# Kernel tuning notes

Measured on AMD Instinct MI355X. Metric: run time of the kernel, lower is better.

Reference implementation:

```python
import jax, jax.numpy as jnp
import numpy as np

NEG_BIG = -9e15

def setup_inputs() -> dict:
    key = jax.random.key(0)
    k1, k2, k3, k4 = jax.random.split(key, 4)
    N, Fin, Fout = 8192, 256, 128
    x = jax.random.normal(k1, (N, Fin), dtype=jnp.float32)
    adj = jax.random.randint(k2, (N, N), 0, 2, dtype=jnp.int32)
    # xavier-uniform-like init
    limW = float(np.sqrt(6.0 / (Fin + Fout)))
    W = jax.random.uniform(k3, (Fin, Fout), minval=-limW, maxval=limW, dtype=jnp.float32)
    lima = float(np.sqrt(6.0 / (2 * Fout + 1)))
    a = jax.random.uniform(k4, (2 * Fout, 1), minval=-lima, maxval=lima, dtype=jnp.float32)
    return {"x": x, "adj": adj, "W": W, "a": a}

def reference(x, adj, W, a, alpha=0.2):
    # h: (N, Fout)
    h = x @ W
    Fout = W.shape[1]
    # Split a into source/target halves: e[i,j] = leakyrelu(h_i·a1 + h_j·a2)
    a1, a2 = a[:Fout, 0], a[Fout:, 0]
    s = h @ a1  # (N,) row (source) scores
    t = h @ a2  # (N,) col (target) scores
    e = jax.nn.leaky_relu(s[:, None] + t[None, :], negative_slope=alpha)  # (N, N)
    e = jnp.where(adj > 0, e, NEG_BIG)
    attention = jax.nn.softmax(e, axis=1)
    # dropout omitted (eval mode / training=False)
    return attention @ h
```

## Files before the change

kernel.cpp:

```cpp
#include <hip/hip_runtime.h>
#include <hip/hip_bf16.h>

typedef __attribute__((ext_vector_type(8))) short short8;
typedef __attribute__((ext_vector_type(4))) short short4v;
typedef __attribute__((ext_vector_type(4))) float f32x4;

#define NR 8192
#define LOG2E 1.4426950408889634f

__device__ __forceinline__ short f2bf(float f) {
  return __builtin_bit_cast(short, __float2bfloat16(f));
}

__global__ __launch_bounds__(256) void k_gemm_h(const float* __restrict__ x,
                                                const float* __restrict__ W,
                                                const float* __restrict__ a,
                                                short* __restrict__ HT2,
                                                float* __restrict__ sv,
                                                float* __restrict__ tv) {
  __shared__ short WT[128][136];
  const int tid = threadIdx.x;
  const int w = tid >> 6;
  const int L = tid & 63;
  const int lm = L & 15;
  const int q = L >> 4;
  const int i0 = blockIdx.x * 64;

  f32x4 acc[8];
#pragma unroll
  for (int nn = 0; nn < 8; ++nn) acc[nn] = (f32x4){0.f, 0.f, 0.f, 0.f};

  for (int kc = 0; kc < 256; kc += 128) {
    if (kc) __syncthreads();
#pragma unroll
    for (int p = 0; p < 16; ++p) {
      int idx = p * 256 + tid;
      int k = idx >> 5;
      int f4 = (idx & 31) * 4;
      float4 v = *(const float4*)&W[(kc + k) * 128 + f4];
      WT[f4 + 0][k] = f2bf(v.x);
      WT[f4 + 1][k] = f2bf(v.y);
      WT[f4 + 2][k] = f2bf(v.z);
      WT[f4 + 3][k] = f2bf(v.w);
    }
    __syncthreads();
#pragma unroll
    for (int ks = 0; ks < 4; ++ks) {
      int row = i0 + 16 * w + lm;
      const float* xp = &x[(size_t)row * 256 + kc + ks * 32 + q * 8];
      float4 xa = *(const float4*)xp;
      float4 xb = *(const float4*)(xp + 4);
      short8 af;
      af[0] = f2bf(xa.x); af[1] = f2bf(xa.y); af[2] = f2bf(xa.z); af[3] = f2bf(xa.w);
      af[4] = f2bf(xb.x); af[5] = f2bf(xb.y); af[6] = f2bf(xb.z); af[7] = f2bf(xb.w);
#pragma unroll
      for (int nn = 0; nn < 8; ++nn) {
        short8 bf = *(const short8*)&WT[nn * 16 + lm][ks * 32 + q * 8];
        acc[nn] = __builtin_amdgcn_mfma_f32_16x16x32_bf16(af, bf, acc[nn], 0, 0, 0);
      }
    }
  }

  const int ib = i0 + 16 * w + 4 * q;
  const int tbase = (ib >> 5) * 4096 + (ib & 31);
  float a1v[8], a2v[8];
#pragma unroll
  for (int nn = 0; nn < 8; ++nn) {
    a1v[nn] = a[nn * 16 + lm];
    a2v[nn] = a[128 + nn * 16 + lm];
  }
  float sr[4] = {0.f, 0.f, 0.f, 0.f};
  float tr[4] = {0.f, 0.f, 0.f, 0.f};
#pragma unroll
  for (int nn = 0; nn < 8; ++nn) {
    int f = nn * 16 + lm;
    short4v o;
    o[0] = f2bf(acc[nn][0]);
    o[1] = f2bf(acc[nn][1]);
    o[2] = f2bf(acc[nn][2]);
    o[3] = f2bf(acc[nn][3]);
    *(short4v*)&HT2[tbase + f * 32] = o;
#pragma unroll
    for (int r = 0; r < 4; ++r) {
      sr[r] += acc[nn][r] * a1v[nn];
      tr[r] += acc[nn][r] * a2v[nn];
    }
  }
#pragma unroll
  for (int d = 1; d < 16; d <<= 1) {
#pragma unroll
    for (int r = 0; r < 4; ++r) {
      sr[r] += __shfl_xor(sr[r], d);
      tr[r] += __shfl_xor(tr[r], d);
    }
  }
  if (lm == 0) {
#pragma unroll
    for (int r = 0; r < 4; ++r) {
      sv[ib + r] = sr[r] * LOG2E;
      tv[ib + r] = tr[r] * LOG2E;
    }
  }
}

__global__ __launch_bounds__(512, 4) void k_flash(const int* __restrict__ adj,
                                                  const short* __restrict__ HT2,
                                                  const float* __restrict__ sv,
                                                  const float* __restrict__ tv,
                                                  float* __restrict__ part,
                                                  float* __restrict__ lpart) {
  __shared__ short lds_s[32768];
  unsigned* ldsw = (unsigned*)lds_s;
  const int tid = threadIdx.x;
  const int w = tid >> 6;
  const int L = tid & 63;
  const int lm = L & 15;
  const int q = L >> 4;
  const int sp = blockIdx.x & 7;
  const int it = blockIdx.x >> 3;
  const int i0 = it * 128;

  const int row0 = i0 + 16 * w + lm;
  const float s0 = sv[row0];
  const size_t ar0 = (size_t)row0 * NR;

  f32x4 acc[8];
#pragma unroll
  for (int nn = 0; nn < 8; ++nn) acc[nn] = (f32x4){0.f, 0.f, 0.f, 0.f};
  float l0 = 0.f;

  const int tile0 = sp * 32;
  int jb = tile0 * 32 + q * 8;
  int4 sa00 = *(const int4*)&adj[ar0 + jb];
  int4 sa01 = *(const int4*)&adj[ar0 + jb + 4];

  for (int t = 0; t < 32; ++t) {
    if ((t & 7) == 0) {
      __syncthreads();
      const int pbase_t = tile0 + t;
#pragma unroll
      for (int z = 0; z < 8; ++z) {
        int id = z * 512 + tid;
        int tt = id >> 9;
        int k = id & 511;
        int f = k >> 2, c = k & 3;
        uint4 v = *(const uint4*)&HT2[(size_t)(pbase_t + tt) * 4096 + k * 8];
        int cs = c ^ ((f >> 1) & 3);
        *(uint4*)&ldsw[tt * 2048 + f * 16 + cs * 4] = v;
      }
      __syncthreads();
    }
    int4 a00 = sa00, a01 = sa01;
    if (t + 1 < 32) {
      int jn = (tile0 + t + 1) * 32 + q * 8;
      sa00 = *(const int4*)&adj[ar0 + jn];
      sa01 = *(const int4*)&adj[ar0 + jn + 4];
    }
    const int jc = (tile0 + t) * 32 + q * 8;
    float4 tv0 = *(const float4*)&tv[jc];
    float4 tv1 = *(const float4*)&tv[jc + 4];
    const int tt = t & 7;
    short8 bf[8];
#pragma unroll
    for (int nn = 0; nn < 8; ++nn) {
      int f = nn * 16 + lm;
      bf[nn] = *(const short8*)&ldsw[tt * 2048 + f * 16 + ((q ^ ((f >> 1) & 3)) * 4)];
    }

    int av0[8] = {a00.x, a00.y, a00.z, a00.w, a01.x, a01.y, a01.z, a01.w};
    float tvl[8] = {tv0.x, tv0.y, tv0.z, tv0.w, tv1.x, tv1.y, tv1.z, tv1.w};
    short8 p0;
#pragma unroll
    for (int e = 0; e < 8; ++e) {
      float v0 = s0 + tvl[e];
      float e0 = fmaxf(v0, 0.2f * v0);
      float pp0 = (av0[e] > 0) ? __builtin_amdgcn_exp2f(e0) : 0.f;
      l0 += pp0;
      p0[e] = f2bf(pp0);
    }
#pragma unroll
    for (int nn = 0; nn < 8; ++nn)
      acc[nn] = __builtin_amdgcn_mfma_f32_16x16x32_bf16(p0, bf[nn], acc[nn], 0, 0, 0);
  }
  __syncthreads();

  float* my = (float*)lds_s + w * 2048;
#pragma unroll
  for (int nn = 0; nn < 8; ++nn)
#pragma unroll
    for (int r = 0; r < 4; ++r)
      my[(4 * q + r) * 128 + nn * 16 + lm] = acc[nn][r];
  float* pbase = part + ((size_t)sp * NR + i0 + 16 * w) * 128;
#pragma unroll
  for (int c = 0; c < 8; ++c) {
    int idx = (c * 64 + L) * 4;
    *(float4*)&pbase[idx] = *(const float4*)&my[idx];
  }

  l0 += __shfl_xor(l0, 16);
  l0 += __shfl_xor(l0, 32);
  if (q == 0) lpart[sp * NR + row0] = l0;
}

__global__ __launch_bounds__(256) void k_reduce(const float* __restrict__ part,
                                                const float* __restrict__ lpart,
                                                float* __restrict__ out, int S) {
  int idx4 = blockIdx.x * 256 + threadIdx.x;
  int idx = idx4 * 4;
  int i = idx >> 7;
  float4 sum = {0.f, 0.f, 0.f, 0.f};
  for (int sp = 0; sp < S; ++sp) {
    float4 v = *(const float4*)&part[(size_t)sp * (NR * 128) + idx];
    sum.x += v.x; sum.y += v.y; sum.z += v.z; sum.w += v.w;
  }
  float l = 0.f;
  for (int sp = 0; sp < S; ++sp) l += lpart[sp * NR + i];
  float inv = (l > 0.f) ? 1.f / l : 0.f;
  float4 o = {sum.x * inv, sum.y * inv, sum.z * inv, sum.w * inv};
  *(float4*)&out[idx] = o;
}

extern "C" void kernel_launch(void* const* d_in, const int* in_sizes, int n_in,
                              void* d_out, int out_size, void* d_ws, size_t ws_size,
                              hipStream_t stream) {
  const float* x = (const float*)d_in[0];
  const int* adj = (const int*)d_in[1];
  const float* W = (const float*)d_in[2];
  const float* a = (const float*)d_in[3];
  float* out = (float*)d_out;

  char* ws = (char*)d_ws;
  short* HT2 = (short*)(ws + 0);
  float* sv = (float*)(ws + 2097152);
  float* tv = (float*)(ws + 2129920);
  float* lpart = (float*)(ws + 2162688);
  float* part = (float*)(ws + 2424832);

  const int S = 8;

  hipLaunchKernelGGL(k_gemm_h, dim3(128), dim3(256), 0, stream, x, W, a, HT2, sv, tv);
  hipLaunchKernelGGL(k_flash, dim3(64 * S), dim3(512), 0, stream, adj, HT2, sv, tv,
                     part, lpart);
  hipLaunchKernelGGL(k_reduce, dim3((NR * 128) / 1024), dim3(256), 0, stream, part,
                     lpart, out, S);
}
```

Before: 431.9 us.

## Fuse split-K reduction into flash kernel via last-block atomic counter

Removes the separate reduce kernel launch. Each row-tile's split blocks increment an atomic counter after writing partials, and the last of the 8 arriving blocks sums the partials and normalizes into the output. The counter is zeroed in the first GEMM kernel. This saves a launch and a full pass scheduling gap, at the cost of threadfences, an atomic per block, and a serialized tail reduce done by one block per row tile.

Measured after the change: 615.5 us. 1.43x slower.

```diff
diff --git a/kernel.cpp b/kernel.cpp
--- a/kernel.cpp
+++ b/kernel.cpp
@@ -17,9 +17,11 @@
                                                 const float* __restrict__ a,
                                                 short* __restrict__ HT2,
                                                 float* __restrict__ sv,
-                                                float* __restrict__ tv) {
+                                                float* __restrict__ tv,
+                                                int* __restrict__ cnt) {
   __shared__ short WT[128][136];
   const int tid = threadIdx.x;
+  if (blockIdx.x == 0 && tid < 64) cnt[tid] = 0;
   const int w = tid >> 6;
   const int L = tid & 63;
   const int lm = L & 15;
@@ -108,7 +110,9 @@
                                                   const float* __restrict__ sv,
                                                   const float* __restrict__ tv,
                                                   float* __restrict__ part,
-                                                  float* __restrict__ lpart) {
+                                                  float* __restrict__ lpart,
+                                                  int* __restrict__ cnt,
+                                                  float* __restrict__ out) {
   __shared__ short lds_s[32768];
   unsigned* ldsw = (unsigned*)lds_s;
   const int tid = threadIdx.x;
@@ -200,24 +204,33 @@
   l0 += __shfl_xor(l0, 16);
   l0 += __shfl_xor(l0, 32);
   if (q == 0) lpart[sp * NR + row0] = l0;
-}
-
-__global__ __launch_bounds__(256) void k_reduce(const float* __restrict__ part,
-                                                const float* __restrict__ lpart,
-                                                float* __restrict__ out, int S) {
-  int idx4 = blockIdx.x * 256 + threadIdx.x;
-  int idx = idx4 * 4;
-  int i = idx >> 7;
-  float4 sum = {0.f, 0.f, 0.f, 0.f};
-  for (int sp = 0; sp < S; ++sp) {
-    float4 v = *(const float4*)&part[(size_t)sp * (NR * 128) + idx];
-    sum.x += v.x; sum.y += v.y; sum.z += v.z; sum.w += v.w;
-  }
-  float l = 0.f;
-  for (int sp = 0; sp < S; ++sp) l += lpart[sp * NR + i];
-  float inv = (l > 0.f) ? 1.f / l : 0.f;
-  float4 o = {sum.x * inv, sum.y * inv, sum.z * inv, sum.w * inv};
-  *(float4*)&out[idx] = o;
+
+  __threadfence();
+  __syncthreads();
+  volatile int* flagp = (volatile int*)lds_s;
+  if (tid == 0) *flagp = (atomicAdd(&cnt[it], 1) == 7) ? 1 : 0;
+  __syncthreads();
+  if (*flagp == 0) return;
+  __threadfence();
+
+  const size_t pb = (size_t)i0 * 128;
+#pragma unroll
+  for (int c = 0; c < 8; ++c) {
+    int e = (c * 512 + tid) * 4;
+    int r = e >> 7;
+    f32x4 sum = (f32x4){0.f, 0.f, 0.f, 0.f};
+    float l = 0.f;
+#pragma unroll
+    for (int spp = 0; spp < 8; ++spp) {
+      const f32x4 v = *(const f32x4*)&part[(size_t)spp * (NR * 128) + pb + e];
+      sum[0] += v[0]; sum[1] += v[1]; sum[2] += v[2]; sum[3] += v[3];
+      l += lpart[spp * NR + i0 + r];
+    }
+    float inv = (l > 0.f) ? 1.f / l : 0.f;
+    f32x4 o;
+    o[0] = sum[0] * inv; o[1] = sum[1] * inv; o[2] = sum[2] * inv; o[3] = sum[3] * inv;
+    *(f32x4*)&out[pb + e] = o;
+  }
 }
 
 extern "C" void kernel_launch(void* const* d_in, const int* in_sizes, int n_in,
@@ -235,12 +248,12 @@
   float* tv = (float*)(ws + 2129920);
   float* lpart = (float*)(ws + 2162688);
   float* part = (float*)(ws + 2424832);
+  int* cnt = (int*)(ws + 35979264);
 
   const int S = 8;
 
-  hipLaunchKernelGGL(k_gemm_h, dim3(128), dim3(256), 0, stream, x, W, a, HT2, sv, tv);
+  hipLaunchKernelGGL(k_gemm_h, dim3(128), dim3(256), 0, stream, x, W, a, HT2, sv, tv,
+                     cnt);
   hipLaunchKernelGGL(k_flash, dim3(64 * S), dim3(512), 0, stream, adj, HT2, sv, tv,
-                     part, lpart);
-  hipLaunchKernelGGL(k_reduce, dim3((NR * 128) / 1024), dim3(256), 0, stream, part,
-                     lpart, out, S);
-}
+                     part, lpart, cnt, out);
+}
```
